# Optimization experiments

Measured on AMD Instinct MI355X. Metric: run time of the kernel, lower is better.

## Reference

```python
import jax, jax.numpy as jnp
import numpy as np
from jax import lax

ACTIVE_TOKENS = 256

def setup_inputs() -> dict:
    key = jax.random.key(0)
    k1, k2, k3, k4, k5 = jax.random.split(key, 5)
    B, L, D, A = 8, 4096, 1024, 256
    return {
        "x": jax.random.normal(k1, (B, L, D), dtype=jnp.float32),
        "active": jax.random.normal(k2, (B, A, D), dtype=jnp.float32),
        "cold": jax.random.normal(k3, (B, D), dtype=jnp.float32),
        "w_sal": jax.random.normal(k4, (D,), dtype=jnp.float32) * 0.02,
        "w_read": jax.random.normal(k5, (D, D), dtype=jnp.float32) * 0.02,
    }

def reference(x, active, cold, w_sal, w_read):
    # combined: [B, A+L, D]
    combined = jnp.concatenate([active, x], axis=1)
    B, Lc, D = combined.shape
    keep = min(ACTIVE_TOKENS, Lc)
    # salience head: Linear(D, 1, bias=False) -> [B, Lc]
    salience = jnp.einsum("bld,d->bl", combined, w_sal)
    _, top_idx = lax.top_k(salience, keep)          # [B, keep]
    top_idx = jnp.sort(top_idx, axis=-1)
    # gather kept tokens; torch detaches new_active before use
    kept = jnp.take_along_axis(combined, top_idx[:, :, None], axis=1)  # [B, keep, D]
    new_active = lax.stop_gradient(kept)
    # dropped-token mean (masked_select compaction == total minus kept)
    n_dropped = Lc - keep  # static > 0 here
    dropped_mean = (combined.sum(axis=1) - kept.sum(axis=1)) / n_dropped  # [B, D]
    cold_new = 0.9 * cold + 0.1 * dropped_mean
    # contexts and residual read projection
    active_ctx = new_active.mean(axis=1)            # [B, D]
    ctx = active_ctx + cold_new                      # [B, D]
    x_out = x + jnp.einsum("bd,ed->be", ctx, w_read)[:, None, :]  # Linear: ctx @ W^T
    return x_out, new_active, lax.stop_gradient(cold_new)
```

## Files before the change

### kernel.cpp

```cpp
#include <hip/hip_runtime.h>

#define B 8
#define XROWS 4096
#define AROWS 256
#define LC 4352
#define DD 1024
#define KEEP 256

__device__ __forceinline__ const float* combined_row(const float* __restrict__ x,
                                                     const float* __restrict__ act,
                                                     int b, int l) {
    return (l < AROWS) ? (act + ((size_t)b * AROWS + l) * DD)
                       : (x + ((size_t)b * XROWS + (l - AROWS)) * DD);
}

__global__ __launch_bounds__(256) void k_zero(float* __restrict__ p, int n) {
    int i = blockIdx.x * 256 + threadIdx.x;
    if (i < n) p[i] = 0.0f;
}

__global__ __launch_bounds__(256) void k_sal_sums(
        const float* __restrict__ x, const float* __restrict__ act,
        const float* __restrict__ wsal, float* __restrict__ sal,
        float* __restrict__ sums) {
    const int tid  = threadIdx.x;
    const int wave = tid >> 6;
    const int lane = tid & 63;
    const int b     = blockIdx.x / 68;
    const int chunk = blockIdx.x % 68;
    const int row0  = chunk * 64;
    const int col   = lane * 16;

    const float4 w0 = *(const float4*)(wsal + col + 0);
    const float4 w1 = *(const float4*)(wsal + col + 4);
    const float4 w2 = *(const float4*)(wsal + col + 8);
    const float4 w3 = *(const float4*)(wsal + col + 12);

    float4 c0 = make_float4(0,0,0,0), c1 = c0, c2 = c0, c3 = c0;

    for (int r = wave; r < 64; r += 4) {
        const int l = row0 + r;
        const float* rp = combined_row(x, act, b, l) + col;
        const float4 a0 = ((const float4*)rp)[0];
        const float4 a1 = ((const float4*)rp)[1];
        const float4 a2 = ((const float4*)rp)[2];
        const float4 a3 = ((const float4*)rp)[3];
        c0.x += a0.x; c0.y += a0.y; c0.z += a0.z; c0.w += a0.w;
        c1.x += a1.x; c1.y += a1.y; c1.z += a1.z; c1.w += a1.w;
        c2.x += a2.x; c2.y += a2.y; c2.z += a2.z; c2.w += a2.w;
        c3.x += a3.x; c3.y += a3.y; c3.z += a3.z; c3.w += a3.w;
        float s = a0.x*w0.x + a0.y*w0.y + a0.z*w0.z + a0.w*w0.w
                + a1.x*w1.x + a1.y*w1.y + a1.z*w1.z + a1.w*w1.w
                + a2.x*w2.x + a2.y*w2.y + a2.z*w2.z + a2.w*w2.w
                + a3.x*w3.x + a3.y*w3.y + a3.z*w3.z + a3.w*w3.w;
        #pragma unroll
        for (int m = 32; m >= 1; m >>= 1) s += __shfl_xor(s, m, 64);
        if (lane == 0) sal[b * LC + l] = s;
    }

    __shared__ float acc[DD];
    for (int k = tid; k < DD; k += 256) acc[k] = 0.0f;
    __syncthreads();
    for (int w = 0; w < 4; ++w) {
        if (wave == w) {
            float* a = acc + col;
            a[0]+=c0.x;  a[1]+=c0.y;  a[2]+=c0.z;  a[3]+=c0.w;
            a[4]+=c1.x;  a[5]+=c1.y;  a[6]+=c1.z;  a[7]+=c1.w;
            a[8]+=c2.x;  a[9]+=c2.y;  a[10]+=c2.z; a[11]+=c2.w;
            a[12]+=c3.x; a[13]+=c3.y; a[14]+=c3.z; a[15]+=c3.w;
        }
        __syncthreads();
    }
    const int c4 = tid * 4;
    float* sb = sums + b * DD;
    atomicAdd(sb + c4 + 0, acc[c4 + 0]);
    atomicAdd(sb + c4 + 1, acc[c4 + 1]);
    atomicAdd(sb + c4 + 2, acc[c4 + 2]);
    atomicAdd(sb + c4 + 3, acc[c4 + 3]);
}

__global__ __launch_bounds__(1024) void k_topk(const float* __restrict__ sal,
                                               int* __restrict__ idx) {
    const int b = blockIdx.x;
    const int tid = threadIdx.x;
    __shared__ unsigned keys[LC];
    __shared__ int scanbuf[1024];
    __shared__ int cntS;

    for (int i = tid; i < LC; i += 1024) {
        unsigned u = __float_as_uint(sal[b * LC + i]);
        keys[i] = (u & 0x80000000u) ? ~u : (u | 0x80000000u);
    }
    __syncthreads();

    unsigned T = 0;
    for (int bit = 31; bit >= 0; --bit) {
        const unsigned cand = T | (1u << bit);
        if (tid == 0) cntS = 0;
        __syncthreads();
        int c = 0;
        for (int i = tid; i < LC; i += 1024) c += (keys[i] >= cand) ? 1 : 0;
        #pragma unroll
        for (int m = 32; m >= 1; m >>= 1) c += __shfl_xor(c, m, 64);
        if ((tid & 63) == 0) atomicAdd(&cntS, c);
        __syncthreads();
        const int cnt = cntS;
        __syncthreads();
        if (cnt >= KEEP) T = cand;
    }

    const int start = tid * 5;
    const int end = (start + 5 < LC) ? (start + 5) : LC;
    int gt = 0, eq = 0;
    for (int i = start; i < end; ++i) {
        if (i < LC) { gt += (keys[i] > T); eq += (keys[i] == T); }
    }
    scanbuf[tid] = (gt << 16) | eq;
    for (int off = 1; off < 1024; off <<= 1) {
        __syncthreads();
        const int v = (tid >= off) ? scanbuf[tid - off] : 0;
        __syncthreads();
        scanbuf[tid] += v;
    }
    __syncthreads();
    const int total   = scanbuf[1023];
    const int incl    = scanbuf[tid];
    const int totalGT = total >> 16;
    const int needEQ  = KEEP - totalGT;
    int gtB = (incl >> 16) - gt;
    int eqB = (incl & 0xFFFF) - eq;
    for (int i = start; i < end; ++i) {
        if (i >= LC) break;
        const unsigned k = keys[i];
        if (k > T) {
            idx[b * KEEP + gtB + min(eqB, needEQ)] = i;
            ++gtB;
        } else if (k == T) {
            if (eqB < needEQ) idx[b * KEEP + gtB + eqB] = i;
            ++eqB;
        }
    }
}

__global__ __launch_bounds__(256) void k_gather(const float* __restrict__ x,
        const float* __restrict__ act, const int* __restrict__ idx,
        float* __restrict__ out_active, float* __restrict__ ksum) {
    const int b = blockIdx.x >> 3;
    const int chunk = blockIdx.x & 7;
    const int tid = threadIdx.x;
    const int c4 = tid * 4;
    float4 cs = make_float4(0,0,0,0);
    for (int r = 0; r < 32; ++r) {
        const int k = chunk * 32 + r;
        const int l = idx[b * KEEP + k];
        const float4 v = *(const float4*)(combined_row(x, act, b, l) + c4);
        *(float4*)(out_active + ((size_t)b * KEEP + k) * DD + c4) = v;
        cs.x += v.x; cs.y += v.y; cs.z += v.z; cs.w += v.w;
    }
    float* kb = ksum + b * DD;
    atomicAdd(kb + c4 + 0, cs.x);
    atomicAdd(kb + c4 + 1, cs.y);
    atomicAdd(kb + c4 + 2, cs.z);
    atomicAdd(kb + c4 + 3, cs.w);
}

__global__ __launch_bounds__(256) void k_ctx(const float* __restrict__ sums,
        const float* __restrict__ ksum, const float* __restrict__ cold,
        float* __restrict__ out_cold, float* __restrict__ ctx) {
    const int i = blockIdx.x * 256 + threadIdx.x;
    const float s = sums[i];
    const float ks = ksum[i];
    const float dm = (s - ks) * (1.0f / 4096.0f);
    const float cn = 0.9f * cold[i] + 0.1f * dm;
    out_cold[i] = cn;
    ctx[i] = ks * (1.0f / 256.0f) + cn;
}

__global__ __launch_bounds__(256) void k_read(const float* __restrict__ ctx,
        const float* __restrict__ wread, float* __restrict__ rvec) {
    const int e = blockIdx.x;
    const int tid = threadIdx.x;
    const int c4 = tid * 4;
    const float4 w = *(const float4*)(wread + (size_t)e * DD + c4);
    float p[B];
    #pragma unroll
    for (int bb = 0; bb < B; ++bb) {
        const float4 c = *(const float4*)(ctx + bb * DD + c4);
        p[bb] = w.x*c.x + w.y*c.y + w.z*c.z + w.w*c.w;
    }
    __shared__ float red[B][256];
    #pragma unroll
    for (int bb = 0; bb < B; ++bb) red[bb][tid] = p[bb];
    __syncthreads();
    for (int s = 128; s > 0; s >>= 1) {
        if (tid < s) {
            #pragma unroll
            for (int bb = 0; bb < B; ++bb) red[bb][tid] += red[bb][tid + s];
        }
        __syncthreads();
    }
    if (tid < B) rvec[tid * DD + e] = red[tid][0];
}

__global__ __launch_bounds__(256) void k_xout(const float* __restrict__ x,
        const float* __restrict__ rvec, float* __restrict__ xout) {
    const size_t total = (size_t)B * XROWS * (DD / 4);
    const float4* x4 = (const float4*)x;
    const float4* r4 = (const float4*)rvec;
    float4* o4 = (float4*)xout;
    for (size_t i = (size_t)blockIdx.x * 256 + threadIdx.x; i < total;
         i += (size_t)gridDim.x * 256) {
        float4 v = x4[i];
        const int e4 = (int)(i & 255);
        const int bb = (int)(i >> 20);
        const float4 r = r4[(bb << 8) | e4];
        v.x += r.x; v.y += r.y; v.z += r.z; v.w += r.w;
        o4[i] = v;
    }
}

extern "C" void kernel_launch(void* const* d_in, const int* in_sizes, int n_in,
                              void* d_out, int out_size, void* d_ws, size_t ws_size,
                              hipStream_t stream) {
    (void)in_sizes; (void)n_in; (void)out_size; (void)ws_size;
    const float* x     = (const float*)d_in[0];
    const float* act   = (const float*)d_in[1];
    const float* cold  = (const float*)d_in[2];
    const float* wsal  = (const float*)d_in[3];
    const float* wread = (const float*)d_in[4];

    float* out        = (float*)d_out;
    float* xout       = out;
    float* out_active = xout + (size_t)B * XROWS * DD;
    float* out_cold   = out_active + (size_t)B * KEEP * DD;

    float* ws   = (float*)d_ws;
    float* sal  = ws;
    float* sums = sal + B * LC;
    float* ksum = sums + B * DD;
    float* ctx  = ksum + B * DD;
    float* rvec = ctx + B * DD;
    int*   idx  = (int*)(rvec + B * DD);

    k_zero<<<(2 * B * DD + 255) / 256, 256, 0, stream>>>(sums, 2 * B * DD);
    k_sal_sums<<<B * 68, 256, 0, stream>>>(x, act, wsal, sal, sums);
    k_topk<<<B, 1024, 0, stream>>>(sal, idx);
    k_gather<<<B * 8, 256, 0, stream>>>(x, act, idx, out_active, ksum);
    k_ctx<<<(B * DD) / 256, 256, 0, stream>>>(sums, ksum, cold, out_cold, ctx);
    k_read<<<DD, 256, 0, stream>>>(ctx, wread, rvec);
    k_xout<<<8192, 256, 0, stream>>>(x, rvec, xout);
}
```

Measured before the change: 324.5 us.

## Radix-select top-k, fuse ctx into read, nontemporal stores, retile salience pass

Replaces the 32-pass bitwise threshold search in top-k with a 4-pass 8-bit radix histogram select, and swaps the block-wide shared scan for wave shuffle scans. Folds the ctx/cold computation into the read-projection kernel, which removes one launch and one buffer. Zeroing of ksum moves into the top-k kernel. The salience/sum pass now uses 32-row chunks with coalesced column mapping and a single-sync reduction. The large output writes use nontemporal stores. Each read block now recomputes ctx for all batches, which adds redundant work.

```diff
diff --git a/kernel.cpp b/kernel.cpp
--- a/kernel.cpp
+++ b/kernel.cpp
@@ -6,6 +6,13 @@
 #define LC 4352
 #define DD 1024
 #define KEEP 256
+
+typedef float vfloat4 __attribute__((ext_vector_type(4)));
+
+__device__ __forceinline__ void nt_store4(const float4& v, float* p) {
+    vfloat4 t = {v.x, v.y, v.z, v.w};
+    __builtin_nontemporal_store(t, (vfloat4*)p);
+}
 
 __device__ __forceinline__ const float* combined_row(const float* __restrict__ x,
                                                      const float* __restrict__ act,
@@ -26,29 +33,29 @@
     const int tid  = threadIdx.x;
     const int wave = tid >> 6;
     const int lane = tid & 63;
-    const int b     = blockIdx.x / 68;
-    const int chunk = blockIdx.x % 68;
-    const int row0  = chunk * 64;
-    const int col   = lane * 16;
-
-    const float4 w0 = *(const float4*)(wsal + col + 0);
-    const float4 w1 = *(const float4*)(wsal + col + 4);
-    const float4 w2 = *(const float4*)(wsal + col + 8);
-    const float4 w3 = *(const float4*)(wsal + col + 12);
-
-    float4 c0 = make_float4(0,0,0,0), c1 = c0, c2 = c0, c3 = c0;
-
-    for (int r = wave; r < 64; r += 4) {
+    const int b     = blockIdx.x / 136;
+    const int chunk = blockIdx.x % 136;
+    const int row0  = chunk * 32;
+    const int c0 = lane * 4;
+
+    const float4 w0 = *(const float4*)(wsal + 0 * 256 + c0);
+    const float4 w1 = *(const float4*)(wsal + 1 * 256 + c0);
+    const float4 w2 = *(const float4*)(wsal + 2 * 256 + c0);
+    const float4 w3 = *(const float4*)(wsal + 3 * 256 + c0);
+
+    float4 s0 = make_float4(0,0,0,0), s1 = s0, s2 = s0, s3 = s0;
+
+    for (int r = wave; r < 32; r += 4) {
         const int l = row0 + r;
-        const float* rp = combined_row(x, act, b, l) + col;
-        const float4 a0 = ((const float4*)rp)[0];
-        const float4 a1 = ((const float4*)rp)[1];
-        const float4 a2 = ((const float4*)rp)[2];
-        const float4 a3 = ((const float4*)rp)[3];
-        c0.x += a0.x; c0.y += a0.y; c0.z += a0.z; c0.w += a0.w;
-        c1.x += a1.x; c1.y += a1.y; c1.z += a1.z; c1.w += a1.w;
-        c2.x += a2.x; c2.y += a2.y; c2.z += a2.z; c2.w += a2.w;
-        c3.x += a3.x; c3.y += a3.y; c3.z += a3.z; c3.w += a3.w;
+        const float* rp = combined_row(x, act, b, l);
+        const float4 a0 = *(const float4*)(rp + 0 * 256 + c0);
+        const float4 a1 = *(const float4*)(rp + 1 * 256 + c0);
+        const float4 a2 = *(const float4*)(rp + 2 * 256 + c0);
+        const float4 a3 = *(const float4*)(rp + 3 * 256 + c0);
+        s0.x += a0.x; s0.y += a0.y; s0.z += a0.z; s0.w += a0.w;
+        s1.x += a1.x; s1.y += a1.y; s1.z += a1.z; s1.w += a1.w;
+        s2.x += a2.x; s2.y += a2.y; s2.z += a2.z; s2.w += a2.w;
+        s3.x += a3.x; s3.y += a3.y; s3.z += a3.z; s3.w += a3.w;
         float s = a0.x*w0.x + a0.y*w0.y + a0.z*w0.z + a0.w*w0.w
                 + a1.x*w1.x + a1.y*w1.y + a1.z*w1.z + a1.w*w1.w
                 + a2.x*w2.x + a2.y*w2.y + a2.z*w2.z + a2.w*w2.w
@@ -58,79 +65,107 @@
         if (lane == 0) sal[b * LC + l] = s;
     }
 
-    __shared__ float acc[DD];
-    for (int k = tid; k < DD; k += 256) acc[k] = 0.0f;
-    __syncthreads();
-    for (int w = 0; w < 4; ++w) {
-        if (wave == w) {
-            float* a = acc + col;
-            a[0]+=c0.x;  a[1]+=c0.y;  a[2]+=c0.z;  a[3]+=c0.w;
-            a[4]+=c1.x;  a[5]+=c1.y;  a[6]+=c1.z;  a[7]+=c1.w;
-            a[8]+=c2.x;  a[9]+=c2.y;  a[10]+=c2.z; a[11]+=c2.w;
-            a[12]+=c3.x; a[13]+=c3.y; a[14]+=c3.z; a[15]+=c3.w;
-        }
-        __syncthreads();
-    }
-    const int c4 = tid * 4;
+    __shared__ float acc[4][DD];
+    float* aw = acc[wave];
+    *(float4*)(aw + 0 * 256 + c0) = s0;
+    *(float4*)(aw + 1 * 256 + c0) = s1;
+    *(float4*)(aw + 2 * 256 + c0) = s2;
+    *(float4*)(aw + 3 * 256 + c0) = s3;
+    __syncthreads();
+    const int col = tid * 4;
+    float4 t0 = *(const float4*)(acc[0] + col);
+    float4 t1 = *(const float4*)(acc[1] + col);
+    float4 t2 = *(const float4*)(acc[2] + col);
+    float4 t3 = *(const float4*)(acc[3] + col);
     float* sb = sums + b * DD;
-    atomicAdd(sb + c4 + 0, acc[c4 + 0]);
-    atomicAdd(sb + c4 + 1, acc[c4 + 1]);
-    atomicAdd(sb + c4 + 2, acc[c4 + 2]);
-    atomicAdd(sb + c4 + 3, acc[c4 + 3]);
+    atomicAdd(sb + col + 0, t0.x + t1.x + t2.x + t3.x);
+    atomicAdd(sb + col + 1, t0.y + t1.y + t2.y + t3.y);
+    atomicAdd(sb + col + 2, t0.z + t1.z + t2.z + t3.z);
+    atomicAdd(sb + col + 3, t0.w + t1.w + t2.w + t3.w);
 }
 
 __global__ __launch_bounds__(1024) void k_topk(const float* __restrict__ sal,
-                                               int* __restrict__ idx) {
+                                               int* __restrict__ idx,
+                                               float* __restrict__ ksum) {
     const int b = blockIdx.x;
     const int tid = threadIdx.x;
+    const int lane = tid & 63;
     __shared__ unsigned keys[LC];
-    __shared__ int scanbuf[1024];
-    __shared__ int cntS;
+    __shared__ int hist[256];
+    __shared__ int wtot4[4];
+    __shared__ int wtot16[16];
+    __shared__ unsigned prefS;
+    __shared__ int kremS;
+
+    if (tid < DD) ksum[b * DD + tid] = 0.0f;
 
     for (int i = tid; i < LC; i += 1024) {
         unsigned u = __float_as_uint(sal[b * LC + i]);
         keys[i] = (u & 0x80000000u) ? ~u : (u | 0x80000000u);
     }
-    __syncthreads();
-
-    unsigned T = 0;
-    for (int bit = 31; bit >= 0; --bit) {
-        const unsigned cand = T | (1u << bit);
-        if (tid == 0) cntS = 0;
-        __syncthreads();
-        int c = 0;
-        for (int i = tid; i < LC; i += 1024) c += (keys[i] >= cand) ? 1 : 0;
-        #pragma unroll
-        for (int m = 32; m >= 1; m >>= 1) c += __shfl_xor(c, m, 64);
-        if ((tid & 63) == 0) atomicAdd(&cntS, c);
-        __syncthreads();
-        const int cnt = cntS;
-        __syncthreads();
-        if (cnt >= KEEP) T = cand;
-    }
+    if (tid == 0) { prefS = 0u; kremS = KEEP; }
+    __syncthreads();
+
+    for (int pass = 0; pass < 4; ++pass) {
+        const int shift = 24 - 8 * pass;
+        if (tid < 256) hist[tid] = 0;
+        __syncthreads();
+        const unsigned pref = prefS;
+        const int krem = kremS;
+        for (int i = tid; i < LC; i += 1024) {
+            const unsigned k = keys[i];
+            if (pass == 0 || (k >> (shift + 8)) == (pref >> (shift + 8)))
+                atomicAdd(&hist[(k >> shift) & 255], 1);
+        }
+        __syncthreads();
+        int h = 0, cum = 0;
+        if (tid < 256) {
+            h = hist[tid];
+            cum = h;
+            #pragma unroll
+            for (int off = 1; off <= 32; off <<= 1) {
+                int v = __shfl_down(cum, off, 64);
+                if (lane + off < 64) cum += v;
+            }
+            if (lane == 0) wtot4[tid >> 6] = cum;
+        }
+        __syncthreads();
+        if (tid < 256) {
+            for (int w2 = (tid >> 6) + 1; w2 < 4; ++w2) cum += wtot4[w2];
+            if (cum >= krem && (cum - h) < krem) {
+                prefS = pref | ((unsigned)tid << shift);
+                kremS = krem - (cum - h);
+            }
+        }
+        __syncthreads();
+    }
+
+    const unsigned T = prefS;
+    const int needEQ = kremS;
 
     const int start = tid * 5;
     const int end = (start + 5 < LC) ? (start + 5) : LC;
     int gt = 0, eq = 0;
     for (int i = start; i < end; ++i) {
-        if (i < LC) { gt += (keys[i] > T); eq += (keys[i] == T); }
-    }
-    scanbuf[tid] = (gt << 16) | eq;
-    for (int off = 1; off < 1024; off <<= 1) {
-        __syncthreads();
-        const int v = (tid >= off) ? scanbuf[tid - off] : 0;
-        __syncthreads();
-        scanbuf[tid] += v;
-    }
-    __syncthreads();
-    const int total   = scanbuf[1023];
-    const int incl    = scanbuf[tid];
-    const int totalGT = total >> 16;
-    const int needEQ  = KEEP - totalGT;
-    int gtB = (incl >> 16) - gt;
-    int eqB = (incl & 0xFFFF) - eq;
+        const unsigned k = keys[i];
+        gt += (k > T);
+        eq += (k == T);
+    }
+    int packed = (gt << 16) | eq;
+    int p = packed;
+    #pragma unroll
+    for (int off = 1; off <= 32; off <<= 1) {
+        int v = __shfl_up(p, off, 64);
+        if (lane >= off) p += v;
+    }
+    if (lane == 63) wtot16[tid >> 6] = p;
+    __syncthreads();
+    int base = 0;
+    for (int w2 = 0; w2 < (tid >> 6); ++w2) base += wtot16[w2];
+    const int exc = p - packed + base;
+    int gtB = exc >> 16;
+    int eqB = exc & 0xFFFF;
     for (int i = start; i < end; ++i) {
-        if (i >= LC) break;
         const unsigned k = keys[i];
         if (k > T) {
             idx[b * KEEP + gtB + min(eqB, needEQ)] = i;
@@ -154,7 +189,7 @@
         const int k = chunk * 32 + r;
         const int l = idx[b * KEEP + k];
         const float4 v = *(const float4*)(combined_row(x, act, b, l) + c4);
-        *(float4*)(out_active + ((size_t)b * KEEP + k) * DD + c4) = v;
+        nt_store4(v, out_active + ((size_t)b * KEEP + k) * DD + c4);
         cs.x += v.x; cs.y += v.y; cs.z += v.z; cs.w += v.w;
     }
     float* kb = ksum + b * DD;
@@ -164,42 +199,52 @@
     atomicAdd(kb + c4 + 3, cs.w);
 }
 
-__global__ __launch_bounds__(256) void k_ctx(const float* __restrict__ sums,
+__global__ __launch_bounds__(256) void k_read(const float* __restrict__ sums,
         const float* __restrict__ ksum, const float* __restrict__ cold,
-        float* __restrict__ out_cold, float* __restrict__ ctx) {
-    const int i = blockIdx.x * 256 + threadIdx.x;
-    const float s = sums[i];
-    const float ks = ksum[i];
-    const float dm = (s - ks) * (1.0f / 4096.0f);
-    const float cn = 0.9f * cold[i] + 0.1f * dm;
-    out_cold[i] = cn;
-    ctx[i] = ks * (1.0f / 256.0f) + cn;
-}
-
-__global__ __launch_bounds__(256) void k_read(const float* __restrict__ ctx,
-        const float* __restrict__ wread, float* __restrict__ rvec) {
+        const float* __restrict__ wread, float* __restrict__ rvec,
+        float* __restrict__ out_cold) {
     const int e = blockIdx.x;
     const int tid = threadIdx.x;
+    const int wave = tid >> 6;
+    const int lane = tid & 63;
     const int c4 = tid * 4;
+    __shared__ float ctxs[B][DD];
+    __shared__ float part[4][B];
+
+    #pragma unroll
+    for (int bb = 0; bb < B; ++bb) {
+        const float4 s  = *(const float4*)(sums + bb * DD + c4);
+        const float4 ks = *(const float4*)(ksum + bb * DD + c4);
+        const float4 cd = *(const float4*)(cold + bb * DD + c4);
+        float4 cn, cx;
+        cn.x = 0.9f * cd.x + 0.1f * ((s.x - ks.x) * (1.0f / 4096.0f));
+        cn.y = 0.9f * cd.y + 0.1f * ((s.y - ks.y) * (1.0f / 4096.0f));
+        cn.z = 0.9f * cd.z + 0.1f * ((s.z - ks.z) * (1.0f / 4096.0f));
+        cn.w = 0.9f * cd.w + 0.1f * ((s.w - ks.w) * (1.0f / 4096.0f));
+        cx.x = ks.x * (1.0f / 256.0f) + cn.x;
+        cx.y = ks.y * (1.0f / 256.0f) + cn.y;
+        cx.z = ks.z * (1.0f / 256.0f) + cn.z;
+        cx.w = ks.w * (1.0f / 256.0f) + cn.w;
+        *(float4*)(&ctxs[bb][c4]) = cx;
+        if (e == 0) *(float4*)(out_cold + bb * DD + c4) = cn;
+    }
+    __syncthreads();
+
     const float4 w = *(const float4*)(wread + (size_t)e * DD + c4);
     float p[B];
     #pragma unroll
     for (int bb = 0; bb < B; ++bb) {
-        const float4 c = *(const float4*)(ctx + bb * DD + c4);
+        const float4 c = *(const float4*)(&ctxs[bb][c4]);
         p[bb] = w.x*c.x + w.y*c.y + w.z*c.z + w.w*c.w;
     }
-    __shared__ float red[B][256];
-    #pragma unroll
-    for (int bb = 0; bb < B; ++bb) red[bb][tid] = p[bb];
-    __syncthreads();
-    for (int s = 128; s > 0; s >>= 1) {
-        if (tid < s) {
-            #pragma unroll
-            for (int bb = 0; bb < B; ++bb) red[bb][tid] += red[bb][tid + s];
-        }
-        __syncthreads();
-    }
-    if (tid < B) rvec[tid * DD + e] = red[tid][0];
+    #pragma unroll
+    for (int bb = 0; bb < B; ++bb) {
+        #pragma unroll
+        for (int m = 32; m >= 1; m >>= 1) p[bb] += __shfl_xor(p[bb], m, 64);
+        if (lane == 0) part[wave][bb] = p[bb];
+    }
+    __syncthreads();
+    if (tid < B) rvec[tid * DD + e] = part[0][tid] + part[1][tid] + part[2][tid] + part[3][tid];
 }
 
 __global__ __launch_bounds__(256) void k_xout(const float* __restrict__ x,
@@ -207,7 +252,7 @@
     const size_t total = (size_t)B * XROWS * (DD / 4);
     const float4* x4 = (const float4*)x;
     const float4* r4 = (const float4*)rvec;
-    float4* o4 = (float4*)xout;
+    float* of = (float*)xout;
     for (size_t i = (size_t)blockIdx.x * 256 + threadIdx.x; i < total;
          i += (size_t)gridDim.x * 256) {
         float4 v = x4[i];
@@ -215,7 +260,7 @@
         const int bb = (int)(i >> 20);
         const float4 r = r4[(bb << 8) | e4];
         v.x += r.x; v.y += r.y; v.z += r.z; v.w += r.w;
-        o4[i] = v;
+        nt_store4(v, of + i * 4);
     }
 }
 
@@ -238,15 +283,13 @@
     float* sal  = ws;
     float* sums = sal + B * LC;
     float* ksum = sums + B * DD;
-    float* ctx  = ksum + B * DD;
-    float* rvec = ctx + B * DD;
+    float* rvec = ksum + B * DD;
     int*   idx  = (int*)(rvec + B * DD);
 
-    k_zero<<<(2 * B * DD + 255) / 256, 256, 0, stream>>>(sums, 2 * B * DD);
-    k_sal_sums<<<B * 68, 256, 0, stream>>>(x, act, wsal, sal, sums);
-    k_topk<<<B, 1024, 0, stream>>>(sal, idx);
+    k_zero<<<(B * DD + 255) / 256, 256, 0, stream>>>(sums, B * DD);
+    k_sal_sums<<<B * 136, 256, 0, stream>>>(x, act, wsal, sal, sums);
+    k_topk<<<B, 1024, 0, stream>>>(sal, idx, ksum);
     k_gather<<<B * 8, 256, 0, stream>>>(x, act, idx, out_active, ksum);
-    k_ctx<<<(B * DD) / 256, 256, 0, stream>>>(sums, ksum, cold, out_cold, ctx);
-    k_read<<<DD, 256, 0, stream>>>(ctx, wread, rvec);
+    k_read<<<DD, 256, 0, stream>>>(sums, ksum, cold, wread, rvec, out_cold);
     k_xout<<<8192, 256, 0, stream>>>(x, rvec, xout);
 }
```

New measurement: 306.2 us. 5.6% less time.
